# Kernel tuning notes

Hardware: AMD Instinct MI355X
Metric: run time of the kernel (lower is better)

Reference implementation:

```python
import jax, jax.numpy as jnp
import numpy as np

EMBED_DIM = 1024
CONTEXT_LEN = 2048
NUM_HEADS = 16
HEAD_DIM = EMBED_DIM // NUM_HEADS
BATCH = 2
SEQ = 2048


def setup_inputs() -> dict:
    key = jax.random.key(0)
    ks = jax.random.split(key, 6)
    s = 1.0 / np.sqrt(EMBED_DIM)
    x = jax.random.normal(ks[0], (BATCH, SEQ, EMBED_DIM), dtype=jnp.float32)
    # nn.Linear weights stored as [out, in]; we keep [in, out] for x @ W
    W_q = jax.random.uniform(ks[1], (EMBED_DIM, EMBED_DIM), jnp.float32, -s, s)
    W_k = jax.random.uniform(ks[2], (EMBED_DIM, EMBED_DIM), jnp.float32, -s, s)
    W_v = jax.random.uniform(ks[3], (EMBED_DIM, EMBED_DIM), jnp.float32, -s, s)
    W_o = jax.random.uniform(ks[4], (EMBED_DIM, EMBED_DIM), jnp.float32, -s, s)
    b_o = jax.random.uniform(ks[5], (EMBED_DIM,), jnp.float32, -s, s)
    return {"x": x, "W_q": W_q, "W_k": W_k, "W_v": W_v, "W_o": W_o, "b_o": b_o}


def reference(x, W_q, W_k, W_v, W_o, b_o):
    b, s, _ = x.shape
    # project and split heads: [b, s, e] -> [b, h, s, d]
    def heads(t):
        return t.reshape(b, s, NUM_HEADS, HEAD_DIM).transpose(0, 2, 1, 3)
    q = heads(x @ W_q)
    k = heads(x @ W_k)
    v = heads(x @ W_v)
    scores = jnp.einsum("bhqd,bhkd->bhqk", q, k)  # full seq x seq scores
    causal = jnp.triu(jnp.ones((s, s), dtype=bool), k=1)
    scores = jnp.where(causal, -jnp.inf, scores)
    attn = jax.nn.softmax(scores / np.sqrt(HEAD_DIM).astype(np.float32), axis=-1)
    ctx = jnp.einsum("bhqk,bhkd->bhqd", attn, v)
    ctx = ctx.transpose(0, 2, 1, 3).reshape(b, s, EMBED_DIM)
    return ctx @ W_o + b_o
```

## Files before the change

### kernel.cpp

```cpp
#include <hip/hip_runtime.h>

#define EMBED 1024
#define SEQL  2048
#define NHEAD 16
#define HDIM  64
#define NBATCH 2
#define MROWS 4096

typedef __attribute__((ext_vector_type(4))) float  f32x4;
typedef __attribute__((ext_vector_type(8))) __bf16 bf16x8;

__device__ __forceinline__ short f2bf(float f){
  union { float f; unsigned u; } x; x.f = f;
  unsigned r = x.u + 0x7fffu + ((x.u >> 16) & 1u);
  return (short)(r >> 16);
}

#define GLDS(gp, lp) __builtin_amdgcn_global_load_lds( \
    (const __attribute__((address_space(1))) void*)(gp), \
    (__attribute__((address_space(3))) void*)(lp), 16, 0, 0)

__global__ __launch_bounds__(256) void cvt_kernel(const float* __restrict__ in,
                                                  short* __restrict__ out, int n){
  int i = (blockIdx.x * 256 + threadIdx.x) * 4;
  if (i >= n) return;
  float4 v = *(const float4*)(in + i);
  short4 o; o.x = f2bf(v.x); o.y = f2bf(v.y); o.z = f2bf(v.z); o.w = f2bf(v.w);
  *(short4*)(out + i) = o;
}

__global__ __launch_bounds__(256) void transpose_kernel(const float* __restrict__ W0,
    const float* __restrict__ W1, const float* __restrict__ W2, const float* __restrict__ W3,
    short* __restrict__ WtAll){
  __shared__ float tile[32][33];
  const int z = blockIdx.z;
  const float* W = (z==0)?W0:(z==1)?W1:(z==2)?W2:W3;
  short* Wt = WtAll + z*(EMBED*EMBED);
  const int bx = blockIdx.x*32, by = blockIdx.y*32;
  const int tx = threadIdx.x & 31, ty = threadIdx.x >> 5;
  #pragma unroll
  for (int i=0;i<32;i+=8) tile[ty+i][tx] = W[(by+ty+i)*EMBED + bx+tx];
  __syncthreads();
  #pragma unroll
  for (int i=0;i<32;i+=8) Wt[(bx+ty+i)*EMBED + by+tx] = f2bf(tile[tx][ty+i]);
}

__device__ __forceinline__ void gemm_tile_128(const short* __restrict__ A,
    const short* __restrict__ Bt, short* As, short* Bs, int m0, int n0, f32x4 acc[4][4]){
  const int tid  = threadIdx.x;
  const int lane = tid & 63;
  const int wid  = tid >> 6;
  const int wrow = (wid >> 1) * 64, wcol = (wid & 1) * 64;
  const int arow = tid >> 2, acol8 = (tid & 3) * 8;
  const int l15 = lane & 15, lg = lane >> 4;

  auto STAGE = [&](int b, int k0){
    short* as = As + b*4096;
    short* bs = Bs + b*4096;
    GLDS(A  + (m0      + arow) * 1024 + k0 + acol8, as + tid*8);
    GLDS(A  + (m0 + 64 + arow) * 1024 + k0 + acol8, as + 2048 + tid*8);
    GLDS(Bt + (n0      + arow) * 1024 + k0 + acol8, bs + tid*8);
    GLDS(Bt + (n0 + 64 + arow) * 1024 + k0 + acol8, bs + 2048 + tid*8);
  };

  STAGE(0, 0);
  __syncthreads();
  int cur = 0;
  for (int k0 = 0; k0 < 1024; k0 += 32){
    if (k0 + 32 < 1024) STAGE(cur ^ 1, k0 + 32);
    const short* as = As + cur*4096;
    const short* bs = Bs + cur*4096;
    bf16x8 a[4], b[4];
    #pragma unroll
    for (int i=0;i<4;++i) a[i] = *(const bf16x8*)(as + (wrow+16*i+l15)*32 + 8*lg);
    #pragma unroll
    for (int j=0;j<4;++j) b[j] = *(const bf16x8*)(bs + (wcol+16*j+l15)*32 + 8*lg);
    #pragma unroll
    for (int i=0;i<4;++i)
      #pragma unroll
      for (int j=0;j<4;++j)
        acc[i][j] = __builtin_amdgcn_mfma_f32_16x16x32_bf16(a[i], b[j], acc[i][j], 0,0,0);
    __syncthreads();
    cur ^= 1;
  }
}

__global__ __launch_bounds__(256) void gemm_qkv_kernel(const short* __restrict__ Xb,
    const short* __restrict__ WtAll, short* __restrict__ Q, short* __restrict__ K,
    short* __restrict__ Vt){
  __shared__ short As[2*4096], Bs[2*4096];
  const int m0 = blockIdx.x*128, n0 = blockIdx.y*128, z = blockIdx.z;
  const short* Bt = WtAll + z*(EMBED*EMBED);
  f32x4 acc[4][4] = {};
  gemm_tile_128(Xb, Bt, As, Bs, m0, n0, acc);
  const int lane = threadIdx.x & 63;
  const int wid  = threadIdx.x >> 6;
  const int wrow = (wid >> 1) * 64, wcol = (wid & 1) * 64;
  const int l15 = lane & 15, lg = lane >> 4;
  short* out = (z==0) ? Q : (z==1) ? K : Vt;
  const float qscl = (z==0) ? (0.125f * 1.44269504f) : 1.0f;
  #pragma unroll
  for (int i=0;i<4;++i)
    #pragma unroll
    for (int j=0;j<4;++j)
      #pragma unroll
      for (int r=0;r<4;++r){
        int m = m0 + wrow + 16*i + 4*lg + r;
        int n = n0 + wcol + 16*j + l15;
        int bb = m >> 11, srow = m & 2047, hh = n >> 6, d = n & 63;
        short v = f2bf(acc[i][j][r] * qscl);
        if (z < 2) out[(((bb<<4)+hh)*SEQL + srow)*HDIM + d] = v;
        else       out[(((bb<<4)+hh)*HDIM + d)*SEQL + srow] = v;
      }
}

__global__ __launch_bounds__(256) void gemm_out_kernel(const short* __restrict__ Ctx,
    const short* __restrict__ WtO, const float* __restrict__ bias, float* __restrict__ out){
  __shared__ short As[2*4096], Bs[2*4096];
  const int m0 = blockIdx.x*128, n0 = blockIdx.y*128;
  f32x4 acc[4][4] = {};
  gemm_tile_128(Ctx, WtO, As, Bs, m0, n0, acc);
  const int lane = threadIdx.x & 63;
  const int wid  = threadIdx.x >> 6;
  const int wrow = (wid >> 1) * 64, wcol = (wid & 1) * 64;
  const int l15 = lane & 15, lg = lane >> 4;
  #pragma unroll
  for (int i=0;i<4;++i)
    #pragma unroll
    for (int j=0;j<4;++j)
      #pragma unroll
      for (int r=0;r<4;++r){
        int m = m0 + wrow + 16*i + 4*lg + r;
        int n = n0 + wcol + 16*j + l15;
        out[m*EMBED + n] = acc[i][j][r] + bias[n];
      }
}

__global__ __launch_bounds__(512, 4) void attn_kernel(const short* __restrict__ Q,
    const short* __restrict__ K, const short* __restrict__ Vt, short* __restrict__ Ctx){
  __shared__ __align__(16) char lds[49152];
  const int tid  = threadIdx.x;
  const int lane = tid & 63;
  const int wid  = tid >> 6;
  const int bid   = blockIdx.x;
  const int xcd   = bid & 7;
  const int i7    = bid >> 3;
  const int bh    = xcd + 8*(i7 & 3);
  const int cidx  = i7 >> 2;
  const int chunk = (cidx < 8) ? cidx : 23 - cidx;
  const int q0blk = chunk * 128;
  const int ntblk = 2*chunk + 2;
  const int q0w   = q0blk + 16*wid;
  const int qlast = q0w + 15;

  const short* Qh  = Q  + bh*(SEQL*HDIM);
  const char*  KhB = (const char*)(K  + bh*(SEQL*HDIM));
  const char*  VhB = (const char*)(Vt + bh*(HDIM*SEQL));
  const int l15 = lane & 15, lg = lane >> 4;
  const int lg20 = 20 * lg;
  const int swE = (l15 & 7) << 3;
  const int swB = (l15 & 7) << 4;
  const int laneRow = lane >> 3;
  const int colSwz  = 16 * ((lane & 7) ^ laneRow);
  const int r0 = 8 * wid;

  const short* qp = Qh + (q0w + l15)*HDIM + 8*lg;
  bf16x8 bq0 = *(const bf16x8*)qp;
  bf16x8 bq1 = *(const bf16x8*)(qp + 32);

  f32x4 acc[4];
  #pragma unroll
  for (int j=0; j<4; ++j) acc[j] = (f32x4){0.f,0.f,0.f,0.f};
  float mrun = -3e30f, lrun = 0.f;

  short* pw = (short*)(lds + 32768 + wid*2048);

  auto STAGE = [&](int b, int t){
    char* kb = lds + b*16384;
    char* vb = kb + 8192;
    const int kv0 = t*64;
    GLDS(KhB + (kv0 + r0 + laneRow)*128 + colSwz, kb + r0*128);
    GLDS(VhB + (r0 + laneRow)*4096 + kv0*2 + colSwz, vb + r0*128);
  };

  STAGE(0, 0);
  __syncthreads();

  int cur = 0;
  for (int t = 0; t < ntblk; ++t){
    const int kv0 = t*64;
    if (t + 1 < ntblk) STAGE(cur ^ 1, t + 1);
    if (kv0 <= qlast){
      const char* kb = lds + cur*16384;
      const char* vb = kb + 8192;
      f32x4 sc[4];
      __builtin_amdgcn_s_setprio(1);
      #pragma unroll
      for (int c=0; c<4; ++c){
        const char* kr = kb + (16*c + l15)*128;
        bf16x8 k0 = *(const bf16x8*)(kr + ((16*lg) ^ swB));
        bf16x8 k1 = *(const bf16x8*)(kr + ((64 + 16*lg) ^ swB));
        f32x4 z = (f32x4){0.f,0.f,0.f,0.f};
        z = __builtin_amdgcn_mfma_f32_16x16x32_bf16(k0, bq0, z, 0,0,0);
        z = __builtin_amdgcn_mfma_f32_16x16x32_bf16(k1, bq1, z, 0,0,0);
        sc[c] = z;
      }
      __builtin_amdgcn_s_setprio(0);
      if (kv0 + 63 > q0w){
        #pragma unroll
        for (int c=0; c<4; ++c)
          #pragma unroll
          for (int r=0; r<4; ++r)
            if (kv0 + 16*c + 4*lg + r > q0w + l15) sc[c][r] = -3e30f;
      }
      float pm = -3e30f;
      #pragma unroll
      for (int c=0; c<4; ++c)
        #pragma unroll
        for (int r=0; r<4; ++r) pm = fmaxf(pm, sc[c][r]);
      pm = fmaxf(pm, __shfl_xor(pm, 16));
      pm = fmaxf(pm, __shfl_xor(pm, 32));
      const int resc = !__all(pm <= mrun);
      float mn = mrun, ss = 1.0f;
      if (resc){
        mn = fmaxf(mrun, pm);
        ss = __builtin_amdgcn_exp2f(mrun - mn);
        mrun = mn;
      }
      float ls = 0.f;
      #pragma unroll
      for (int c=0; c<4; ++c)
        #pragma unroll
        for (int r=0; r<4; ++r){
          float p = __builtin_amdgcn_exp2f(sc[c][r] - mn);
          sc[c][r] = p;
          ls += p;
        }
      ls += __shfl_xor(ls, 16);
      ls += __shfl_xor(ls, 32);
      if (resc){
        lrun = lrun*ss + ls;
        float srg[4];
        #pragma unroll
        for (int r=0; r<4; ++r) srg[r] = __shfl(ss, lg20 + r);
        #pragma unroll
        for (int j=0; j<4; ++j)
          #pragma unroll
          for (int r=0; r<4; ++r) acc[j][r] *= srg[r];
      } else {
        lrun += ls;
      }
      #pragma unroll
      for (int c=0; c<4; ++c){
        short4 pk;
        pk.x = f2bf(sc[c][0]); pk.y = f2bf(sc[c][1]);
        pk.z = f2bf(sc[c][2]); pk.w = f2bf(sc[c][3]);
        *(short4*)(pw + l15*64 + ((16*c + 4*lg) ^ swE)) = pk;
      }
      bf16x8 pa0 = *(const bf16x8*)(pw + l15*64 + ((8*lg)      ^ swE));
      bf16x8 pa1 = *(const bf16x8*)(pw + l15*64 + ((32 + 8*lg) ^ swE));
      __builtin_amdgcn_s_setprio(1);
      #pragma unroll
      for (int j=0; j<4; ++j){
        const char* vrp = vb + (16*j + l15)*128;
        bf16x8 v0 = *(const bf16x8*)(vrp + ((16*lg) ^ swB));
        bf16x8 v1 = *(const bf16x8*)(vrp + ((64 + 16*lg) ^ swB));
        acc[j] = __builtin_amdgcn_mfma_f32_16x16x32_bf16(pa0, v0, acc[j], 0,0,0);
        acc[j] = __builtin_amdgcn_mfma_f32_16x16x32_bf16(pa1, v1, acc[j], 0,0,0);
      }
      __builtin_amdgcn_s_setprio(0);
    }
    __syncthreads();
    cur ^= 1;
  }

  const int bb = bh >> 4, hh = bh & 15;
  float lr[4];
  #pragma unroll
  for (int r=0; r<4; ++r) lr[r] = __builtin_amdgcn_rcpf(__shfl(lrun, lg20 + r));
  #pragma unroll
  for (int j=0; j<4; ++j)
    #pragma unroll
    for (int r=0; r<4; ++r){
      int qg = q0w + 4*lg + r;
      Ctx[(bb*SEQL + qg)*EMBED + hh*HDIM + 16*j + l15] = f2bf(acc[j][r] * lr[r]);
    }
}

extern "C" void kernel_launch(void* const* d_in, const int* in_sizes, int n_in,
                              void* d_out, int out_size, void* d_ws, size_t ws_size,
                              hipStream_t stream){
  const float* x  = (const float*)d_in[0];
  const float* Wq = (const float*)d_in[1];
  const float* Wk = (const float*)d_in[2];
  const float* Wv = (const float*)d_in[3];
  const float* Wo = (const float*)d_in[4];
  const float* bo = (const float*)d_in[5];
  float* out = (float*)d_out;

  char* ws = (char*)d_ws;
  const size_t MB = 1u << 20;
  short* Xb  = (short*)(ws +  0*MB);
  short* Wt  = (short*)(ws +  8*MB);
  short* Q   = (short*)(ws + 16*MB);
  short* Kk  = (short*)(ws + 24*MB);
  short* Vt  = (short*)(ws + 32*MB);
  short* Ctx = (short*)(ws + 40*MB);

  cvt_kernel<<<4096, 256, 0, stream>>>(x, Xb, MROWS*EMBED);
  transpose_kernel<<<dim3(32,32,4), 256, 0, stream>>>(Wq, Wk, Wv, Wo, Wt);
  gemm_qkv_kernel<<<dim3(32,8,3), 256, 0, stream>>>(Xb, Wt, Q, Kk, Vt);
  attn_kernel<<<512, 512, 0, stream>>>(Q, Kk, Vt, Ctx);
  gemm_out_kernel<<<dim3(32,8), 256, 0, stream>>>(Ctx, Wt + 3*(EMBED*EMBED), bo, out);
}
```

Measured before the change: 113.1 us.

## Stage V-transpose epilogue through LDS and use 64-row tiles for output GEMM

The QKV GEMM epilogue for V now packs each accumulator fragment into a swizzled LDS tile, then writes the transposed Vt with coalesced 16-byte stores. Before, each thread made scattered 2-byte stores along the sequence stride. The output projection GEMM moves to a 64x128 tile, doubling the grid from 256 to 512 blocks to improve occupancy across the CUs. Each block in that GEMM now does less work, so B tiles are reloaded more often.

```diff
diff --git a/kernel.cpp b/kernel.cpp
--- a/kernel.cpp
+++ b/kernel.cpp
@@ -85,47 +85,114 @@
   }
 }
 
+__device__ __forceinline__ void gemm_tile_64(const short* __restrict__ A,
+    const short* __restrict__ Bt, short* As, short* Bs, int m0, int n0, f32x4 acc[2][4]){
+  const int tid  = threadIdx.x;
+  const int lane = tid & 63;
+  const int wid  = tid >> 6;
+  const int wrow = (wid >> 1) * 32, wcol = (wid & 1) * 64;
+  const int arow = tid >> 2, acol8 = (tid & 3) * 8;
+  const int l15 = lane & 15, lg = lane >> 4;
+
+  auto STAGE = [&](int b, int k0){
+    short* as = As + b*2048;
+    short* bs = Bs + b*4096;
+    GLDS(A  + (m0      + arow) * 1024 + k0 + acol8, as + tid*8);
+    GLDS(Bt + (n0      + arow) * 1024 + k0 + acol8, bs + tid*8);
+    GLDS(Bt + (n0 + 64 + arow) * 1024 + k0 + acol8, bs + 2048 + tid*8);
+  };
+
+  STAGE(0, 0);
+  __syncthreads();
+  int cur = 0;
+  for (int k0 = 0; k0 < 1024; k0 += 32){
+    if (k0 + 32 < 1024) STAGE(cur ^ 1, k0 + 32);
+    const short* as = As + cur*2048;
+    const short* bs = Bs + cur*4096;
+    bf16x8 a[2], b[4];
+    #pragma unroll
+    for (int i=0;i<2;++i) a[i] = *(const bf16x8*)(as + (wrow+16*i+l15)*32 + 8*lg);
+    #pragma unroll
+    for (int j=0;j<4;++j) b[j] = *(const bf16x8*)(bs + (wcol+16*j+l15)*32 + 8*lg);
+    #pragma unroll
+    for (int i=0;i<2;++i)
+      #pragma unroll
+      for (int j=0;j<4;++j)
+        acc[i][j] = __builtin_amdgcn_mfma_f32_16x16x32_bf16(a[i], b[j], acc[i][j], 0,0,0);
+    __syncthreads();
+    cur ^= 1;
+  }
+}
+
 __global__ __launch_bounds__(256) void gemm_qkv_kernel(const short* __restrict__ Xb,
     const short* __restrict__ WtAll, short* __restrict__ Q, short* __restrict__ K,
     short* __restrict__ Vt){
-  __shared__ short As[2*4096], Bs[2*4096];
+  __shared__ __align__(16) short SH[16384];
+  short* As = SH;
+  short* Bs = SH + 8192;
   const int m0 = blockIdx.x*128, n0 = blockIdx.y*128, z = blockIdx.z;
   const short* Bt = WtAll + z*(EMBED*EMBED);
   f32x4 acc[4][4] = {};
   gemm_tile_128(Xb, Bt, As, Bs, m0, n0, acc);
+  const int tid  = threadIdx.x;
+  const int lane = tid & 63;
+  const int wid  = tid >> 6;
+  const int wrow = (wid >> 1) * 64, wcol = (wid & 1) * 64;
+  const int l15 = lane & 15, lg = lane >> 4;
+  const int bb = m0 >> 11, srow0 = m0 & 2047;
+
+  if (z < 2){
+    short* out = z ? K : Q;
+    const float qscl = (z==0) ? (0.125f * 1.44269504f) : 1.0f;
+    #pragma unroll
+    for (int i=0;i<4;++i)
+      #pragma unroll
+      for (int j=0;j<4;++j)
+        #pragma unroll
+        for (int r=0;r<4;++r){
+          int m = m0 + wrow + 16*i + 4*lg + r;
+          int n = n0 + wcol + 16*j + l15;
+          int srow = m & 2047, hh = n >> 6, d = n & 63;
+          out[(((bb<<4)+hh)*SEQL + srow)*HDIM + d] = f2bf(acc[i][j][r] * qscl);
+        }
+  } else {
+    short* T = SH;
+    #pragma unroll
+    for (int i=0;i<4;++i)
+      #pragma unroll
+      for (int j=0;j<4;++j){
+        int n_loc = wcol + 16*j + l15;
+        int mb    = wrow + 16*i + 4*lg;
+        short4 pk;
+        pk.x = f2bf(acc[i][j][0]); pk.y = f2bf(acc[i][j][1]);
+        pk.z = f2bf(acc[i][j][2]); pk.w = f2bf(acc[i][j][3]);
+        *(short4*)(T + n_loc*128 + (mb ^ ((n_loc & 7) << 3))) = pk;
+      }
+    __syncthreads();
+    #pragma unroll
+    for (int it=0; it<8; ++it){
+      int n_loc = 16*it + (tid >> 4);
+      int mch   = (tid & 15) * 8;
+      int4 v = *(const int4*)(T + n_loc*128 + (mch ^ ((n_loc & 7) << 3)));
+      int n_glob = n0 + n_loc;
+      int hh = n_glob >> 6, d = n_glob & 63;
+      *(int4*)(Vt + (((bb<<4)+hh)*HDIM + d)*SEQL + srow0 + mch) = v;
+    }
+  }
+}
+
+__global__ __launch_bounds__(256) void gemm_out_kernel(const short* __restrict__ Ctx,
+    const short* __restrict__ WtO, const float* __restrict__ bias, float* __restrict__ out){
+  __shared__ __align__(16) short As[2*2048], Bs[2*4096];
+  const int m0 = blockIdx.x*64, n0 = blockIdx.y*128;
+  f32x4 acc[2][4] = {};
+  gemm_tile_64(Ctx, WtO, As, Bs, m0, n0, acc);
   const int lane = threadIdx.x & 63;
   const int wid  = threadIdx.x >> 6;
-  const int wrow = (wid >> 1) * 64, wcol = (wid & 1) * 64;
-  const int l15 = lane & 15, lg = lane >> 4;
-  short* out = (z==0) ? Q : (z==1) ? K : Vt;
-  const float qscl = (z==0) ? (0.125f * 1.44269504f) : 1.0f;
-  #pragma unroll
-  for (int i=0;i<4;++i)
-    #pragma unroll
-    for (int j=0;j<4;++j)
-      #pragma unroll
-      for (int r=0;r<4;++r){
-        int m = m0 + wrow + 16*i + 4*lg + r;
-        int n = n0 + wcol + 16*j + l15;
-        int bb = m >> 11, srow = m & 2047, hh = n >> 6, d = n & 63;
-        short v = f2bf(acc[i][j][r] * qscl);
-        if (z < 2) out[(((bb<<4)+hh)*SEQL + srow)*HDIM + d] = v;
-        else       out[(((bb<<4)+hh)*HDIM + d)*SEQL + srow] = v;
-      }
-}
-
-__global__ __launch_bounds__(256) void gemm_out_kernel(const short* __restrict__ Ctx,
-    const short* __restrict__ WtO, const float* __restrict__ bias, float* __restrict__ out){
-  __shared__ short As[2*4096], Bs[2*4096];
-  const int m0 = blockIdx.x*128, n0 = blockIdx.y*128;
-  f32x4 acc[4][4] = {};
-  gemm_tile_128(Ctx, WtO, As, Bs, m0, n0, acc);
-  const int lane = threadIdx.x & 63;
-  const int wid  = threadIdx.x >> 6;
-  const int wrow = (wid >> 1) * 64, wcol = (wid & 1) * 64;
-  const int l15 = lane & 15, lg = lane >> 4;
-  #pragma unroll
-  for (int i=0;i<4;++i)
+  const int wrow = (wid >> 1) * 32, wcol = (wid & 1) * 64;
+  const int l15 = lane & 15, lg = lane >> 4;
+  #pragma unroll
+  for (int i=0;i<2;++i)
     #pragma unroll
     for (int j=0;j<4;++j)
       #pragma unroll
@@ -311,5 +378,5 @@
   transpose_kernel<<<dim3(32,32,4), 256, 0, stream>>>(Wq, Wk, Wv, Wo, Wt);
   gemm_qkv_kernel<<<dim3(32,8,3), 256, 0, stream>>>(Xb, Wt, Q, Kk, Vt);
   attn_kernel<<<512, 512, 0, stream>>>(Q, Kk, Vt, Ctx);
-  gemm_out_kernel<<<dim3(32,8), 256, 0, stream>>>(Ctx, Wt + 3*(EMBED*EMBED), bo, out);
-}
+  gemm_out_kernel<<<dim3(64,8), 256, 0, stream>>>(Ctx, Wt + 3*(EMBED*EMBED), bo, out);
+}
```

After: 112.2 us. No clear change (-0.8%).
